# Kernel optimization log

Hardware: AMD Instinct MI355X
Metric: run time of the kernel (lower is better)

The kernel has to match this reference:

```python
import jax, jax.numpy as jnp
import numpy as np


def setup_inputs() -> dict:
    key = jax.random.key(0)
    kq, kk, kv, km = jax.random.split(key, 4)
    B, H, S, DK, DV = 2, 16, 2048, 64, 64
    q = jax.random.normal(kq, (B, H, S, DK), dtype=jnp.float32)
    k = jax.random.normal(kk, (B, H, S, DK), dtype=jnp.float32)
    v = jax.random.normal(kv, (B, H, S, DV), dtype=jnp.float32)
    mask = jax.random.randint(km, (B, 1, S, S), 0, 2).astype(bool)
    return {"q": q, "k": k, "v": v, "mask": mask}


def reference(q, k, v, mask):
    d_k = k.shape[3]
    # score: (B, H, Sq, Sk)
    score = jnp.einsum("bhqd,bhkd->bhqk", q, k) / jnp.sqrt(jnp.float32(d_k))
    if mask is not None:
        # Faithful to original: masked positions set to 1e-9 (not -inf)
        score = jnp.where(mask == 0, jnp.asarray(1e-9, score.dtype), score)
    attention = jax.nn.softmax(score, axis=-1)
    context = jnp.einsum("bhqk,bhkd->bhqd", attention, v)
    return (context, attention)
```

## Files before the change

### kernel.cpp

```cpp
#include <hip/hip_runtime.h>


#define S_LEN 2048
#define DKV 64
#define NBH 32
#define NH 16
#define TILE 64
#define PAD 4

__global__ __launch_bounds__(256) void attn_p_kernel(
    const float* __restrict__ q, const float* __restrict__ k,
    const int* __restrict__ mask, float* __restrict__ attn,
    float* __restrict__ rowsum)
{
    __shared__ float Qts[TILE][TILE + PAD];
    __shared__ float Kts[TILE][TILE + PAD];

    const int kt = blockIdx.x;
    const int qt = blockIdx.y;
    const int bh = blockIdx.z;
    const int t  = threadIdx.x;
    const int tx = t & 15;
    const int ty = t >> 4;

    const float* qbase = q + (size_t)(bh * S_LEN + qt * TILE) * DKV;
    const float* kbase = k + (size_t)(bh * S_LEN + kt * TILE) * DKV;
#pragma unroll
    for (int j = 0; j < 4; ++j) {
        const int f   = (t + 256 * j) * 4;
        const int row = f >> 6;
        const int c   = f & 63;
        const float4 a4 = *(const float4*)(qbase + f);
        Qts[c + 0][row] = a4.x; Qts[c + 1][row] = a4.y;
        Qts[c + 2][row] = a4.z; Qts[c + 3][row] = a4.w;
        const float4 b4 = *(const float4*)(kbase + f);
        Kts[c + 0][row] = b4.x; Kts[c + 1][row] = b4.y;
        Kts[c + 2][row] = b4.z; Kts[c + 3][row] = b4.w;
    }
    __syncthreads();

    float acc[4][4] = {};
#pragma unroll 8
    for (int kk = 0; kk < 64; ++kk) {
        const float4 a4 = *(const float4*)&Qts[kk][4 * ty];
        const float4 b4 = *(const float4*)&Kts[kk][4 * tx];
        const float a[4] = {a4.x, a4.y, a4.z, a4.w};
        const float b[4] = {b4.x, b4.y, b4.z, b4.w};
#pragma unroll
        for (int i = 0; i < 4; ++i)
#pragma unroll
            for (int j = 0; j < 4; ++j)
                acc[i][j] = fmaf(a[i], b[j], acc[i][j]);
    }

    const float scale = 0.125f;
    const int b_idx = bh >> 4;
    const int kc = kt * TILE + 4 * tx;
    float partial[4];
#pragma unroll
    for (int i = 0; i < 4; ++i) {
        const int qr = qt * TILE + 4 * ty + i;
        const int4 m4 = *(const int4*)(mask + (size_t)b_idx * S_LEN * S_LEN
                                            + (size_t)qr * S_LEN + kc);
        float s0 = acc[i][0] * scale; if (m4.x == 0) s0 = 1e-9f;
        float s1 = acc[i][1] * scale; if (m4.y == 0) s1 = 1e-9f;
        float s2 = acc[i][2] * scale; if (m4.z == 0) s2 = 1e-9f;
        float s3 = acc[i][3] * scale; if (m4.w == 0) s3 = 1e-9f;
        float4 p4;
        p4.x = __expf(s0); p4.y = __expf(s1); p4.z = __expf(s2); p4.w = __expf(s3);
        *(float4*)(attn + ((size_t)(bh * S_LEN) + qr) * S_LEN + kc) = p4;
        partial[i] = (p4.x + p4.y) + (p4.z + p4.w);
    }
#pragma unroll
    for (int i = 0; i < 4; ++i) {
#pragma unroll
        for (int off = 8; off > 0; off >>= 1)
            partial[i] += __shfl_down(partial[i], off, 16);
    }
    if (tx == 0) {
#pragma unroll
        for (int i = 0; i < 4; ++i)
            atomicAdd(&rowsum[bh * S_LEN + qt * TILE + 4 * ty + i], partial[i]);
    }
}

__global__ __launch_bounds__(256) void attn_ctx_kernel(
    const float* __restrict__ v, float* __restrict__ attn,
    const float* __restrict__ rowsum, float* __restrict__ ctx)
{
    __shared__ float Pts[TILE][TILE + PAD];
    __shared__ float Vs[TILE][TILE + PAD];
    __shared__ float rinv[TILE];

    const int qt = blockIdx.x;
    const int bh = blockIdx.y;
    const int t  = threadIdx.x;
    const int tx = t & 15;
    const int ty = t >> 4;

    if (t < TILE)
        rinv[t] = 1.0f / rowsum[bh * S_LEN + qt * TILE + t];
    __syncthreads();

    float acc[4][4] = {};
    for (int kt = 0; kt < S_LEN / TILE; ++kt) {
        const float* vbase = v + (size_t)(bh * S_LEN + kt * TILE) * DKV;
#pragma unroll
        for (int j = 0; j < 4; ++j) {
            const int f   = (t + 256 * j) * 4;
            const int row = f >> 6;
            const int c   = f & 63;
            float* pp = attn + ((size_t)(bh * S_LEN) + qt * TILE + row) * S_LEN
                             + kt * TILE + c;
            float4 p4 = *(const float4*)pp;
            const float r = rinv[row];
            p4.x *= r; p4.y *= r; p4.z *= r; p4.w *= r;
            *(float4*)pp = p4;
            Pts[c + 0][row] = p4.x; Pts[c + 1][row] = p4.y;
            Pts[c + 2][row] = p4.z; Pts[c + 3][row] = p4.w;
            *(float4*)&Vs[row][c] = *(const float4*)(vbase + f);
        }
        __syncthreads();
#pragma unroll 8
        for (int kk = 0; kk < 64; ++kk) {
            const float4 a4 = *(const float4*)&Pts[kk][4 * ty];
            const float4 b4 = *(const float4*)&Vs[kk][4 * tx];
            const float a[4] = {a4.x, a4.y, a4.z, a4.w};
            const float b[4] = {b4.x, b4.y, b4.z, b4.w};
#pragma unroll
            for (int i = 0; i < 4; ++i)
#pragma unroll
                for (int j = 0; j < 4; ++j)
                    acc[i][j] = fmaf(a[i], b[j], acc[i][j]);
        }
        __syncthreads();
    }

#pragma unroll
    for (int i = 0; i < 4; ++i) {
        const int qr = qt * TILE + 4 * ty + i;
        float4 c4;
        c4.x = acc[i][0]; c4.y = acc[i][1]; c4.z = acc[i][2]; c4.w = acc[i][3];
        *(float4*)(ctx + ((size_t)(bh * S_LEN) + qr) * DKV + 4 * tx) = c4;
    }
}

extern "C" void kernel_launch(void* const* d_in, const int* in_sizes, int n_in,
                              void* d_out, int out_size, void* d_ws, size_t ws_size,
                              hipStream_t stream) {
    const float* q    = (const float*)d_in[0];
    const float* k    = (const float*)d_in[1];
    const float* v    = (const float*)d_in[2];
    const int*   mask = (const int*)d_in[3];

    float* out  = (float*)d_out;
    float* ctx  = out;
    float* attn = out + (size_t)NBH * S_LEN * DKV;
    float* rowsum = (float*)d_ws;

    hipMemsetAsync(rowsum, 0, (size_t)NBH * S_LEN * sizeof(float), stream);

    attn_p_kernel<<<dim3(S_LEN / TILE, S_LEN / TILE, NBH), 256, 0, stream>>>(
        q, k, mask, attn, rowsum);
    attn_ctx_kernel<<<dim3(S_LEN / TILE, NBH), 256, 0, stream>>>(
        v, attn, rowsum, ctx);
}
```

Measured before the change: 1.078 ms.

## Enlarge tiles to 128 and raise per-thread register blocking in both kernels

The score kernel now processes 128x128 tiles with 8x8 outputs per thread, and the context kernel uses 128-row query tiles with 128 threads each computing an 8x8 block of outputs. The aim is to cut shared-memory traffic per FMA and reduce redundant global loads of Q/K/V. In the context kernel each thread rescales its own attention row directly, which removes the shared rinv buffer and one barrier. The cost is higher register pressure and fewer blocks, with the context kernel dropping to 512 blocks of 128 threads, which may lower occupancy. Access to the attention rows in the context kernel is also no longer coalesced, since each thread now walks its own row.

```diff
diff --git a/kernel.cpp b/kernel.cpp
--- a/kernel.cpp
+++ b/kernel.cpp
@@ -2,146 +2,172 @@
 
 
 #define S_LEN 2048
-#define DKV 64
-#define NBH 32
-#define NH 16
-#define TILE 64
-#define PAD 4
+#define DKV   64
+#define NBH   32
+#define TP    128
+#define LSTR  (TP + 4)
+#define CTP   128
 
 __global__ __launch_bounds__(256) void attn_p_kernel(
     const float* __restrict__ q, const float* __restrict__ k,
     const int* __restrict__ mask, float* __restrict__ attn,
     float* __restrict__ rowsum)
 {
-    __shared__ float Qts[TILE][TILE + PAD];
-    __shared__ float Kts[TILE][TILE + PAD];
+    __shared__ float Qts[DKV][LSTR];
+    __shared__ float Kts[DKV][LSTR];
 
     const int kt = blockIdx.x;
     const int qt = blockIdx.y;
     const int bh = blockIdx.z;
     const int t  = threadIdx.x;
+
+    {
+        const int row = t & 127;
+        const int ch  = (t >> 7) * 32;
+        const float* qr = q + ((size_t)(bh * S_LEN + qt * TP + row)) * DKV + ch;
+        const float* kr = k + ((size_t)(bh * S_LEN + kt * TP + row)) * DKV + ch;
+#pragma unroll
+        for (int j = 0; j < 8; ++j) {
+            const int c = ch + 4 * j;
+            const float4 a4 = *(const float4*)(qr + 4 * j);
+            Qts[c + 0][row] = a4.x; Qts[c + 1][row] = a4.y;
+            Qts[c + 2][row] = a4.z; Qts[c + 3][row] = a4.w;
+            const float4 b4 = *(const float4*)(kr + 4 * j);
+            Kts[c + 0][row] = b4.x; Kts[c + 1][row] = b4.y;
+            Kts[c + 2][row] = b4.z; Kts[c + 3][row] = b4.w;
+        }
+    }
+    __syncthreads();
+
     const int tx = t & 15;
     const int ty = t >> 4;
 
-    const float* qbase = q + (size_t)(bh * S_LEN + qt * TILE) * DKV;
-    const float* kbase = k + (size_t)(bh * S_LEN + kt * TILE) * DKV;
+    float acc0[8][4] = {};
+    float acc1[8][4] = {};
+#pragma unroll 8
+    for (int kk = 0; kk < DKV; ++kk) {
+        const float4 a40 = *(const float4*)&Qts[kk][8 * ty];
+        const float4 a41 = *(const float4*)&Qts[kk][8 * ty + 4];
+        const float4 b40 = *(const float4*)&Kts[kk][4 * tx];
+        const float4 b41 = *(const float4*)&Kts[kk][64 + 4 * tx];
+        const float a[8]  = {a40.x, a40.y, a40.z, a40.w, a41.x, a41.y, a41.z, a41.w};
+        const float b0[4] = {b40.x, b40.y, b40.z, b40.w};
+        const float b1[4] = {b41.x, b41.y, b41.z, b41.w};
 #pragma unroll
-    for (int j = 0; j < 4; ++j) {
-        const int f   = (t + 256 * j) * 4;
-        const int row = f >> 6;
-        const int c   = f & 63;
-        const float4 a4 = *(const float4*)(qbase + f);
-        Qts[c + 0][row] = a4.x; Qts[c + 1][row] = a4.y;
-        Qts[c + 2][row] = a4.z; Qts[c + 3][row] = a4.w;
-        const float4 b4 = *(const float4*)(kbase + f);
-        Kts[c + 0][row] = b4.x; Kts[c + 1][row] = b4.y;
-        Kts[c + 2][row] = b4.z; Kts[c + 3][row] = b4.w;
-    }
-    __syncthreads();
-
-    float acc[4][4] = {};
-#pragma unroll 8
-    for (int kk = 0; kk < 64; ++kk) {
-        const float4 a4 = *(const float4*)&Qts[kk][4 * ty];
-        const float4 b4 = *(const float4*)&Kts[kk][4 * tx];
-        const float a[4] = {a4.x, a4.y, a4.z, a4.w};
-        const float b[4] = {b4.x, b4.y, b4.z, b4.w};
+        for (int i = 0; i < 8; ++i) {
 #pragma unroll
-        for (int i = 0; i < 4; ++i)
-#pragma unroll
-            for (int j = 0; j < 4; ++j)
-                acc[i][j] = fmaf(a[i], b[j], acc[i][j]);
+            for (int jj = 0; jj < 4; ++jj) {
+                acc0[i][jj] = fmaf(a[i], b0[jj], acc0[i][jj]);
+                acc1[i][jj] = fmaf(a[i], b1[jj], acc1[i][jj]);
+            }
+        }
     }
 
     const float scale = 0.125f;
     const int b_idx = bh >> 4;
-    const int kc = kt * TILE + 4 * tx;
-    float partial[4];
+    const int c0 = kt * TP + 4 * tx;
+    const int c1 = c0 + 64;
+    float partial[8];
 #pragma unroll
-    for (int i = 0; i < 4; ++i) {
-        const int qr = qt * TILE + 4 * ty + i;
-        const int4 m4 = *(const int4*)(mask + (size_t)b_idx * S_LEN * S_LEN
-                                            + (size_t)qr * S_LEN + kc);
-        float s0 = acc[i][0] * scale; if (m4.x == 0) s0 = 1e-9f;
-        float s1 = acc[i][1] * scale; if (m4.y == 0) s1 = 1e-9f;
-        float s2 = acc[i][2] * scale; if (m4.z == 0) s2 = 1e-9f;
-        float s3 = acc[i][3] * scale; if (m4.w == 0) s3 = 1e-9f;
-        float4 p4;
-        p4.x = __expf(s0); p4.y = __expf(s1); p4.z = __expf(s2); p4.w = __expf(s3);
-        *(float4*)(attn + ((size_t)(bh * S_LEN) + qr) * S_LEN + kc) = p4;
-        partial[i] = (p4.x + p4.y) + (p4.z + p4.w);
+    for (int i = 0; i < 8; ++i) {
+        const int qr = qt * TP + 8 * ty + i;
+        const int* mrow = mask + (size_t)b_idx * S_LEN * S_LEN + (size_t)qr * S_LEN;
+        const int4 m0 = *(const int4*)(mrow + c0);
+        const int4 m1 = *(const int4*)(mrow + c1);
+        float s;
+        float4 p0, p1;
+        s = acc0[i][0] * scale; if (m0.x == 0) s = 1e-9f; p0.x = __expf(s);
+        s = acc0[i][1] * scale; if (m0.y == 0) s = 1e-9f; p0.y = __expf(s);
+        s = acc0[i][2] * scale; if (m0.z == 0) s = 1e-9f; p0.z = __expf(s);
+        s = acc0[i][3] * scale; if (m0.w == 0) s = 1e-9f; p0.w = __expf(s);
+        s = acc1[i][0] * scale; if (m1.x == 0) s = 1e-9f; p1.x = __expf(s);
+        s = acc1[i][1] * scale; if (m1.y == 0) s = 1e-9f; p1.y = __expf(s);
+        s = acc1[i][2] * scale; if (m1.z == 0) s = 1e-9f; p1.z = __expf(s);
+        s = acc1[i][3] * scale; if (m1.w == 0) s = 1e-9f; p1.w = __expf(s);
+        float* arow = attn + ((size_t)(bh * S_LEN) + qr) * S_LEN;
+        *(float4*)(arow + c0) = p0;
+        *(float4*)(arow + c1) = p1;
+        partial[i] = ((p0.x + p0.y) + (p0.z + p0.w))
+                   + ((p1.x + p1.y) + (p1.z + p1.w));
     }
 #pragma unroll
-    for (int i = 0; i < 4; ++i) {
+    for (int i = 0; i < 8; ++i) {
 #pragma unroll
         for (int off = 8; off > 0; off >>= 1)
             partial[i] += __shfl_down(partial[i], off, 16);
     }
     if (tx == 0) {
+        const int rbase = bh * S_LEN + qt * TP + 8 * ty;
 #pragma unroll
-        for (int i = 0; i < 4; ++i)
-            atomicAdd(&rowsum[bh * S_LEN + qt * TILE + 4 * ty + i], partial[i]);
+        for (int i = 0; i < 8; ++i)
+            atomicAdd(&rowsum[rbase + i], partial[i]);
     }
 }
 
-__global__ __launch_bounds__(256) void attn_ctx_kernel(
+__global__ __launch_bounds__(128) void attn_ctx_kernel(
     const float* __restrict__ v, float* __restrict__ attn,
     const float* __restrict__ rowsum, float* __restrict__ ctx)
 {
-    __shared__ float Pts[TILE][TILE + PAD];
-    __shared__ float Vs[TILE][TILE + PAD];
-    __shared__ float rinv[TILE];
+    __shared__ float Pts[DKV][LSTR];
+    __shared__ float Vs[DKV][DKV + 4];
 
     const int qt = blockIdx.x;
     const int bh = blockIdx.y;
     const int t  = threadIdx.x;
-    const int tx = t & 15;
-    const int ty = t >> 4;
+    const int tx = t & 7;
+    const int ty = t >> 3;
 
-    if (t < TILE)
-        rinv[t] = 1.0f / rowsum[bh * S_LEN + qt * TILE + t];
-    __syncthreads();
+    const float rinv = 1.0f / rowsum[bh * S_LEN + qt * CTP + t];
+    float* prow = attn + ((size_t)(bh * S_LEN) + qt * CTP + t) * S_LEN;
 
-    float acc[4][4] = {};
-    for (int kt = 0; kt < S_LEN / TILE; ++kt) {
-        const float* vbase = v + (size_t)(bh * S_LEN + kt * TILE) * DKV;
+    float acc[8][8] = {};
+    for (int kt = 0; kt < S_LEN / DKV; ++kt) {
 #pragma unroll
-        for (int j = 0; j < 4; ++j) {
-            const int f   = (t + 256 * j) * 4;
-            const int row = f >> 6;
-            const int c   = f & 63;
-            float* pp = attn + ((size_t)(bh * S_LEN) + qt * TILE + row) * S_LEN
-                             + kt * TILE + c;
-            float4 p4 = *(const float4*)pp;
-            const float r = rinv[row];
-            p4.x *= r; p4.y *= r; p4.z *= r; p4.w *= r;
-            *(float4*)pp = p4;
-            Pts[c + 0][row] = p4.x; Pts[c + 1][row] = p4.y;
-            Pts[c + 2][row] = p4.z; Pts[c + 3][row] = p4.w;
-            *(float4*)&Vs[row][c] = *(const float4*)(vbase + f);
+        for (int j = 0; j < 16; ++j) {
+            float4 p4 = *(const float4*)(prow + kt * DKV + 4 * j);
+            p4.x *= rinv; p4.y *= rinv; p4.z *= rinv; p4.w *= rinv;
+            *(float4*)(prow + kt * DKV + 4 * j) = p4;
+            const int c = 4 * j;
+            Pts[c + 0][t] = p4.x; Pts[c + 1][t] = p4.y;
+            Pts[c + 2][t] = p4.z; Pts[c + 3][t] = p4.w;
+        }
+        const float* vbase = v + (size_t)(bh * S_LEN + kt * DKV) * DKV;
+#pragma unroll
+        for (int j = 0; j < 8; ++j) {
+            const int f  = (t + 128 * j) * 4;
+            const int vr = f >> 6;
+            const int vc = f & 63;
+            *(float4*)&Vs[vr][vc] = *(const float4*)(vbase + f);
         }
         __syncthreads();
+
 #pragma unroll 8
-        for (int kk = 0; kk < 64; ++kk) {
-            const float4 a4 = *(const float4*)&Pts[kk][4 * ty];
-            const float4 b4 = *(const float4*)&Vs[kk][4 * tx];
-            const float a[4] = {a4.x, a4.y, a4.z, a4.w};
-            const float b[4] = {b4.x, b4.y, b4.z, b4.w};
+        for (int kk = 0; kk < DKV; ++kk) {
+            const float4 a40 = *(const float4*)&Pts[kk][8 * ty];
+            const float4 a41 = *(const float4*)&Pts[kk][8 * ty + 4];
+            const float4 b40 = *(const float4*)&Vs[kk][8 * tx];
+            const float4 b41 = *(const float4*)&Vs[kk][8 * tx + 4];
+            const float a[8] = {a40.x, a40.y, a40.z, a40.w, a41.x, a41.y, a41.z, a41.w};
+            const float b[8] = {b40.x, b40.y, b40.z, b40.w, b41.x, b41.y, b41.z, b41.w};
 #pragma unroll
-            for (int i = 0; i < 4; ++i)
+            for (int i = 0; i < 8; ++i) {
 #pragma unroll
-                for (int j = 0; j < 4; ++j)
-                    acc[i][j] = fmaf(a[i], b[j], acc[i][j]);
+                for (int jj = 0; jj < 8; ++jj)
+                    acc[i][jj] = fmaf(a[i], b[jj], acc[i][jj]);
+            }
         }
         __syncthreads();
     }
 
 #pragma unroll
-    for (int i = 0; i < 4; ++i) {
-        const int qr = qt * TILE + 4 * ty + i;
-        float4 c4;
-        c4.x = acc[i][0]; c4.y = acc[i][1]; c4.z = acc[i][2]; c4.w = acc[i][3];
-        *(float4*)(ctx + ((size_t)(bh * S_LEN) + qr) * DKV + 4 * tx) = c4;
+    for (int i = 0; i < 8; ++i) {
+        const int qr = qt * CTP + 8 * ty + i;
+        float4 c40, c41;
+        c40.x = acc[i][0]; c40.y = acc[i][1]; c40.z = acc[i][2]; c40.w = acc[i][3];
+        c41.x = acc[i][4]; c41.y = acc[i][5]; c41.z = acc[i][6]; c41.w = acc[i][7];
+        float* crow = ctx + ((size_t)(bh * S_LEN) + qr) * DKV + 8 * tx;
+        *(float4*)(crow + 0) = c40;
+        *(float4*)(crow + 4) = c41;
     }
 }
 
@@ -160,8 +186,8 @@
 
     hipMemsetAsync(rowsum, 0, (size_t)NBH * S_LEN * sizeof(float), stream);
 
-    attn_p_kernel<<<dim3(S_LEN / TILE, S_LEN / TILE, NBH), 256, 0, stream>>>(
+    attn_p_kernel<<<dim3(S_LEN / TP, S_LEN / TP, NBH), 256, 0, stream>>>(
         q, k, mask, attn, rowsum);
-    attn_ctx_kernel<<<dim3(S_LEN / TILE, NBH), 256, 0, stream>>>(
+    attn_ctx_kernel<<<dim3(S_LEN / CTP, NBH), 128, 0, stream>>>(
         v, attn, rowsum, ctx);
 }
```

Result: slower. 1.174 ms (+8.9%).
